# Kernel optimization log

Hardware: AMD Instinct MI355X
Metric: run time of the kernel (lower is better)

Reference implementation:

```python
import jax, jax.numpy as jnp
import numpy as np

N_NODES = 50000


def graph_conv(src, dst, x, W, b, n_nodes):
    """DGL GraphConv, norm='both': D_out^{-1/2} A D_in^{-1/2} x W + b.
    src/dst: [E] edge endpoints (message flows src -> dst).
    """
    ones = jnp.ones(src.shape[0], dtype=x.dtype)
    deg_out = jnp.clip(jax.ops.segment_sum(ones, src, num_segments=n_nodes), 1.0)
    deg_in = jnp.clip(jax.ops.segment_sum(ones, dst, num_segments=n_nodes), 1.0)
    h = x * jax.lax.rsqrt(deg_out)[:, None]          # src-side normalization
    msgs = h[src]                                     # [E, F] gather (irregular)
    agg = jax.ops.segment_sum(msgs, dst, num_segments=n_nodes)  # SpMM scatter-add
    agg = agg * jax.lax.rsqrt(deg_in)[:, None]        # dst-side normalization
    return agg @ W + b


def setup_inputs() -> dict:
    key = jax.random.key(0)
    ks = jax.random.split(key, 9)
    E = 600000
    in_f, hid, emb = 128, 64, 32
    features = jax.random.normal(ks[0], (N_NODES, in_f), dtype=jnp.float32)
    src = jax.random.randint(ks[1], (E,), 0, N_NODES)
    dst = jax.random.randint(ks[2], (E,), 0, N_NODES)

    def glorot(k, fan_in, fan_out):
        lim = np.sqrt(6.0 / (fan_in + fan_out)).astype(np.float32)
        return jax.random.uniform(k, (fan_in, fan_out), jnp.float32, -lim, lim)

    return {
        "features": features, "src": src, "dst": dst,
        "W1": glorot(ks[3], in_f, hid), "b1": jnp.zeros((hid,), jnp.float32),
        "W2": glorot(ks[4], hid, emb), "b2": jnp.zeros((emb,), jnp.float32),
        "W3": glorot(ks[5], emb, in_f), "b3": jnp.zeros((in_f,), jnp.float32),
    }


def reference(features, src, dst, W1, b1, W2, b2, W3, b3):
    h = jax.nn.relu(graph_conv(src, dst, features, W1, b1, N_NODES))
    z = graph_conv(src, dst, h, W2, b2, N_NODES)
    recon = graph_conv(src, dst, z, W3, b3, N_NODES)
    return (z, recon)
```

## Files before the change

kernel.cpp:

```cpp
#include <hip/hip_runtime.h>
#include <hip/hip_bf16.h>


#define HNB 4
#define HPB 64
#define HBIN 12500
typedef unsigned short u16;

__device__ __forceinline__ float bfhi(unsigned u) {
    unsigned v = u & 0xFFFF0000u;
    return __builtin_bit_cast(float, v);
}
__device__ __forceinline__ float bflo(unsigned u) {
    unsigned v = u << 16;
    return __builtin_bit_cast(float, v);
}
__device__ __forceinline__ unsigned f2bf(float f) {
    unsigned u = __builtin_bit_cast(unsigned, f);
    return (u + 0x7FFFu + ((u >> 16) & 1u)) >> 16;
}

__global__ __launch_bounds__(256) void k_hist2(
    const int* __restrict__ src, const int* __restrict__ dst,
    u16* __restrict__ slab, int E, int slice)
{
    __shared__ int h[HBIN];
    const int which = blockIdx.x / (HNB * HPB);
    const int bin   = (blockIdx.x / HPB) % HNB;
    const int p     = blockIdx.x % HPB;
    const int* __restrict__ idx = which ? dst : src;

    for (int i = threadIdx.x; i < HBIN; i += 256) h[i] = 0;
    __syncthreads();

    const int lo  = bin * HBIN;
    const int beg = p * slice;
    const int fin = min(beg + slice, E);
    for (int i = beg + threadIdx.x * 4; i + 3 < fin; i += 1024) {
        const int4 v = *(const int4*)(idx + i);
        int u;
        u = v.x - lo; if ((unsigned)u < (unsigned)HBIN) atomicAdd(&h[u], 1);
        u = v.y - lo; if ((unsigned)u < (unsigned)HBIN) atomicAdd(&h[u], 1);
        u = v.z - lo; if ((unsigned)u < (unsigned)HBIN) atomicAdd(&h[u], 1);
        u = v.w - lo; if ((unsigned)u < (unsigned)HBIN) atomicAdd(&h[u], 1);
    }
    for (int i = beg + ((fin - beg) & ~3) + threadIdx.x; i < fin; i += 256) {
        int u = idx[i] - lo;
        if ((unsigned)u < (unsigned)HBIN) atomicAdd(&h[u], 1);
    }
    __syncthreads();

    unsigned* out = (unsigned*)(slab + (size_t)blockIdx.x * HBIN);
    for (int i = threadIdx.x; i < HBIN / 2; i += 256)
        out[i] = (unsigned)h[2 * i] | ((unsigned)h[2 * i + 1] << 16);
}

__global__ __launch_bounds__(256) void k_reduce_scan(
    u16* __restrict__ slab, float* __restrict__ rs_out, float* __restrict__ rs_in,
    int* __restrict__ partial, int* __restrict__ blocksum, int N)
{
    __shared__ int tmp[256];
    const int tid = threadIdx.x;
    const int i = blockIdx.x * 256 + tid;

    int run = 0;
    if (i < N) {
        const int bin = i / HBIN;
        const int off = i - bin * HBIN;
        const u16* s_src = slab + ((size_t)(bin * HPB)) * HBIN + off;
        u16*       s_dst = slab + ((size_t)((HNB + bin) * HPB)) * HBIN + off;

        int so = 0;
#pragma unroll
        for (int p = 0; p < HPB; ++p) so += s_src[(size_t)p * HBIN];
#pragma unroll
        for (int p = 0; p < HPB; ++p) {
            const int c = s_dst[(size_t)p * HBIN];
            s_dst[(size_t)p * HBIN] = (u16)run;
            run += c;
        }
        rs_out[i] = rsqrtf(fmaxf((float)so, 1.0f));
        rs_in[i]  = rsqrtf(fmaxf((float)run, 1.0f));
    }
    tmp[tid] = run; __syncthreads();
    for (int off = 1; off < 256; off <<= 1) {
        int t = (tid >= off) ? tmp[tid - off] : 0;
        __syncthreads(); tmp[tid] += t; __syncthreads();
    }
    if (i < N) partial[i] = tmp[tid];
    if (tid == 255) blocksum[blockIdx.x] = tmp[255];
}

__global__ void k_scan2(int* __restrict__ blocksum, int nb) {
    __shared__ int tmp[256];
    const int tid = threadIdx.x;
    int v = (tid < nb) ? blocksum[tid] : 0;
    tmp[tid] = v; __syncthreads();
    for (int off = 1; off < 256; off <<= 1) {
        int t = (tid >= off) ? tmp[tid - off] : 0;
        __syncthreads(); tmp[tid] += t; __syncthreads();
    }
    if (tid < nb) blocksum[tid] = tmp[tid];
}

__global__ void k_scan3(const int* __restrict__ partial, const int* __restrict__ blocksum,
                        int* __restrict__ row_ptr, int n) {
    const int i = blockIdx.x * 256 + threadIdx.x;
    if (i < n) {
        const int base = (blockIdx.x > 0) ? blocksum[blockIdx.x - 1] : 0;
        row_ptr[i + 1] = partial[i] + base;
        if (i == 0) row_ptr[0] = 0;
    }
}

__global__ __launch_bounds__(256) void k_fill2(
    const int* __restrict__ src, const int* __restrict__ dst,
    const int* __restrict__ row_ptr, const u16* __restrict__ slab,
    int* __restrict__ csr_src, int E, int slice, int N)
{
    __shared__ int cur[HBIN];
    const int bin = blockIdx.x / HPB;
    const int p   = blockIdx.x % HPB;
    const int lo  = bin * HBIN;

    const u16* part_off = slab + ((size_t)((HNB + bin) * HPB + p)) * HBIN;
    for (int j = threadIdx.x; j < HBIN; j += 256) {
        const int node = lo + j;
        cur[j] = (node < N) ? (row_ptr[node] + (int)part_off[j]) : 0;
    }
    __syncthreads();

    const int beg = p * slice;
    const int fin = min(beg + slice, E);
    for (int i = beg + threadIdx.x * 4; i + 3 < fin; i += 1024) {
        const int4 d = *(const int4*)(dst + i);
        const int4 s = *(const int4*)(src + i);
        int u;
        u = d.x - lo; if ((unsigned)u < (unsigned)HBIN) csr_src[atomicAdd(&cur[u], 1)] = s.x;
        u = d.y - lo; if ((unsigned)u < (unsigned)HBIN) csr_src[atomicAdd(&cur[u], 1)] = s.y;
        u = d.z - lo; if ((unsigned)u < (unsigned)HBIN) csr_src[atomicAdd(&cur[u], 1)] = s.z;
        u = d.w - lo; if ((unsigned)u < (unsigned)HBIN) csr_src[atomicAdd(&cur[u], 1)] = s.w;
    }
    for (int i = beg + ((fin - beg) & ~3) + threadIdx.x; i < fin; i += 256) {
        int u = dst[i] - lo;
        if ((unsigned)u < (unsigned)HBIN) csr_src[atomicAdd(&cur[u], 1)] = src[i];
    }
}

template <int IN_F, int OUT_F, int TM>
__global__ __launch_bounds__(256) void k_gemm_bf16out(
    const float* __restrict__ X, const float* __restrict__ W,
    const float* __restrict__ rowscale, u16* __restrict__ Y, int n)
{
    constexpr int CT  = OUT_F / 4;
    constexpr int RT  = 256 / CT;
    constexpr int RPT = TM / RT;
    constexpr int XS  = IN_F + 4;
    __shared__ float sW[IN_F * OUT_F];
    __shared__ float sX[TM * XS];
    const int tid = threadIdx.x;
    const int row0 = blockIdx.x * TM;

    for (int i = tid; i < IN_F * OUT_F / 4; i += 256)
        ((float4*)sW)[i] = ((const float4*)W)[i];
    for (int i = tid; i < TM * IN_F / 4; i += 256) {
        const int r  = i / (IN_F / 4);
        const int c4 = (i % (IN_F / 4)) * 4;
        const int gr = row0 + r;
        float4 v = make_float4(0.f, 0.f, 0.f, 0.f);
        if (gr < n) v = *(const float4*)(X + (long)gr * IN_F + c4);
        *(float4*)(sX + r * XS + c4) = v;
    }
    __syncthreads();

    const int tc = tid % CT;
    const int tr = tid / CT;
    float4 acc[RPT];
#pragma unroll
    for (int i = 0; i < RPT; ++i) acc[i] = make_float4(0.f, 0.f, 0.f, 0.f);

#pragma unroll 8
    for (int k = 0; k < IN_F; ++k) {
        const float4 w = *(const float4*)(sW + k * OUT_F + 4 * tc);
#pragma unroll
        for (int i = 0; i < RPT; ++i) {
            const float xv = sX[(tr + i * RT) * XS + k];
            acc[i].x += xv * w.x; acc[i].y += xv * w.y;
            acc[i].z += xv * w.z; acc[i].w += xv * w.w;
        }
    }

#pragma unroll
    for (int i = 0; i < RPT; ++i) {
        const int gr = row0 + tr + i * RT;
        if (gr < n) {
            float4 v = acc[i];
            const float s = rowscale[gr];
            v.x *= s; v.y *= s; v.z *= s; v.w *= s;
            uint2 pk;
            pk.x = f2bf(v.x) | (f2bf(v.y) << 16);
            pk.y = f2bf(v.z) | (f2bf(v.w) << 16);
            *(uint2*)(Y + (size_t)gr * OUT_F + 4 * tc) = pk;
        }
    }
}

__global__ __launch_bounds__(256) void k_gather_gemm_B(
    const int* __restrict__ row_ptr, const int* __restrict__ csr_src,
    const u16* __restrict__ t1b, const float* __restrict__ rs_in,
    const float* __restrict__ rs_out, const float* __restrict__ b1,
    const float* __restrict__ W2, u16* __restrict__ t2b, int N)
{
    __shared__ float sh[32][72];
    __shared__ float sW[64 * 32];
    const int tid = threadIdx.x;

    for (int i = tid; i < 64 * 32 / 4; i += 256)
        ((float4*)sW)[i] = ((const float4*)W2)[i];

    const int nloc = tid / 8;
    const int node = blockIdx.x * 32 + nloc;
    const int c8 = (tid % 8) * 8;

    float a[8];
#pragma unroll
    for (int t = 0; t < 8; ++t) a[t] = 0.f;

    if (node < N) {
        const int beg = row_ptr[node];
        const int end = row_ptr[node + 1];
        int j = beg;
        for (; j + 3 < end; j += 4) {
            const int s0 = csr_src[j], s1 = csr_src[j + 1];
            const int s2 = csr_src[j + 2], s3 = csr_src[j + 3];
            const uint4 q0 = *(const uint4*)(t1b + (size_t)s0 * 64 + c8);
            const uint4 q1 = *(const uint4*)(t1b + (size_t)s1 * 64 + c8);
            const uint4 q2 = *(const uint4*)(t1b + (size_t)s2 * 64 + c8);
            const uint4 q3 = *(const uint4*)(t1b + (size_t)s3 * 64 + c8);
            a[0] += bflo(q0.x); a[1] += bfhi(q0.x); a[2] += bflo(q0.y); a[3] += bfhi(q0.y);
            a[4] += bflo(q0.z); a[5] += bfhi(q0.z); a[6] += bflo(q0.w); a[7] += bfhi(q0.w);
            a[0] += bflo(q1.x); a[1] += bfhi(q1.x); a[2] += bflo(q1.y); a[3] += bfhi(q1.y);
            a[4] += bflo(q1.z); a[5] += bfhi(q1.z); a[6] += bflo(q1.w); a[7] += bfhi(q1.w);
            a[0] += bflo(q2.x); a[1] += bfhi(q2.x); a[2] += bflo(q2.y); a[3] += bfhi(q2.y);
            a[4] += bflo(q2.z); a[5] += bfhi(q2.z); a[6] += bflo(q2.w); a[7] += bfhi(q2.w);
            a[0] += bflo(q3.x); a[1] += bfhi(q3.x); a[2] += bflo(q3.y); a[3] += bfhi(q3.y);
            a[4] += bflo(q3.z); a[5] += bfhi(q3.z); a[6] += bflo(q3.w); a[7] += bfhi(q3.w);
        }
        for (; j < end; ++j) {
            const int s = csr_src[j];
            const uint4 q = *(const uint4*)(t1b + (size_t)s * 64 + c8);
            a[0] += bflo(q.x); a[1] += bfhi(q.x); a[2] += bflo(q.y); a[3] += bfhi(q.y);
            a[4] += bflo(q.z); a[5] += bfhi(q.z); a[6] += bflo(q.w); a[7] += bfhi(q.w);
        }
        const float rs = rs_in[node];
#pragma unroll
        for (int t = 0; t < 8; ++t)
            a[t] = fmaxf(a[t] * rs + b1[c8 + t], 0.f);
    }
#pragma unroll
    for (int t = 0; t < 8; ++t) sh[nloc][c8 + t] = a[t];
    __syncthreads();

    const int n2 = tid / 8;
    const int c4 = (tid % 8) * 4;
    float4 acc = make_float4(0.f, 0.f, 0.f, 0.f);
#pragma unroll 8
    for (int k = 0; k < 64; ++k) {
        const float xv = sh[n2][k];
        const float4 w = *(const float4*)(sW + k * 32 + c4);
        acc.x += xv * w.x; acc.y += xv * w.y; acc.z += xv * w.z; acc.w += xv * w.w;
    }
    const int gn = blockIdx.x * 32 + n2;
    if (gn < N) {
        const float s = rs_out[gn];
        uint2 pk;
        pk.x = f2bf(acc.x * s) | (f2bf(acc.y * s) << 16);
        pk.y = f2bf(acc.z * s) | (f2bf(acc.w * s) << 16);
        *(uint2*)(t2b + (size_t)gn * 32 + c4) = pk;
    }
}

__global__ __launch_bounds__(256) void k_gather_C(
    const int* __restrict__ row_ptr, const int* __restrict__ csr_src,
    const u16* __restrict__ t2b, const float* __restrict__ rs_in,
    const float* __restrict__ rs_out, const float* __restrict__ b2,
    float* __restrict__ z, u16* __restrict__ zb, int N)
{
    const int node = blockIdx.x * 64 + threadIdx.x / 4;
    const int c8 = (threadIdx.x % 4) * 8;
    if (node >= N) return;

    const int beg = row_ptr[node];
    const int end = row_ptr[node + 1];
    float a[8];
#pragma unroll
    for (int t = 0; t < 8; ++t) a[t] = 0.f;

    int j = beg;
    for (; j + 3 < end; j += 4) {
        const int s0 = csr_src[j], s1 = csr_src[j + 1];
        const int s2 = csr_src[j + 2], s3 = csr_src[j + 3];
        const uint4 q0 = *(const uint4*)(t2b + (size_t)s0 * 32 + c8);
        const uint4 q1 = *(const uint4*)(t2b + (size_t)s1 * 32 + c8);
        const uint4 q2 = *(const uint4*)(t2b + (size_t)s2 * 32 + c8);
        const uint4 q3 = *(const uint4*)(t2b + (size_t)s3 * 32 + c8);
        a[0] += bflo(q0.x); a[1] += bfhi(q0.x); a[2] += bflo(q0.y); a[3] += bfhi(q0.y);
        a[4] += bflo(q0.z); a[5] += bfhi(q0.z); a[6] += bflo(q0.w); a[7] += bfhi(q0.w);
        a[0] += bflo(q1.x); a[1] += bfhi(q1.x); a[2] += bflo(q1.y); a[3] += bfhi(q1.y);
        a[4] += bflo(q1.z); a[5] += bfhi(q1.z); a[6] += bflo(q1.w); a[7] += bfhi(q1.w);
        a[0] += bflo(q2.x); a[1] += bfhi(q2.x); a[2] += bflo(q2.y); a[3] += bfhi(q2.y);
        a[4] += bflo(q2.z); a[5] += bfhi(q2.z); a[6] += bflo(q2.w); a[7] += bfhi(q2.w);
        a[0] += bflo(q3.x); a[1] += bfhi(q3.x); a[2] += bflo(q3.y); a[3] += bfhi(q3.y);
        a[4] += bflo(q3.z); a[5] += bfhi(q3.z); a[6] += bflo(q3.w); a[7] += bfhi(q3.w);
    }
    for (; j < end; ++j) {
        const int s = csr_src[j];
        const uint4 q = *(const uint4*)(t2b + (size_t)s * 32 + c8);
        a[0] += bflo(q.x); a[1] += bfhi(q.x); a[2] += bflo(q.y); a[3] += bfhi(q.y);
        a[4] += bflo(q.z); a[5] += bfhi(q.z); a[6] += bflo(q.w); a[7] += bfhi(q.w);
    }

    const float rs = rs_in[node];
    float v[8];
#pragma unroll
    for (int t = 0; t < 8; ++t) v[t] = a[t] * rs + b2[c8 + t];

    float* o = z + (size_t)node * 32 + c8;
    *(float4*)(o)     = make_float4(v[0], v[1], v[2], v[3]);
    *(float4*)(o + 4) = make_float4(v[4], v[5], v[6], v[7]);

    const float ss = rs_out[node];
    uint4 pk;
    pk.x = f2bf(v[0] * ss) | (f2bf(v[1] * ss) << 16);
    pk.y = f2bf(v[2] * ss) | (f2bf(v[3] * ss) << 16);
    pk.z = f2bf(v[4] * ss) | (f2bf(v[5] * ss) << 16);
    pk.w = f2bf(v[6] * ss) | (f2bf(v[7] * ss) << 16);
    *(uint4*)(zb + (size_t)node * 32 + c8) = pk;
}

__global__ __launch_bounds__(256) void k_gather_gemm_D(
    const int* __restrict__ row_ptr, const int* __restrict__ csr_src,
    const u16* __restrict__ zb, const float* __restrict__ rs_in,
    const float* __restrict__ W3, const float* __restrict__ b3,
    float* __restrict__ recon, int N)
{
    __shared__ float sa[64][36];
    __shared__ float sW[32 * 128];
    const int tid = threadIdx.x;

    for (int i = tid; i < 32 * 128 / 4; i += 256)
        ((float4*)sW)[i] = ((const float4*)W3)[i];

    const int nloc = tid / 4;
    const int node = blockIdx.x * 64 + nloc;
    const int c8 = (tid % 4) * 8;

    float a[8];
#pragma unroll
    for (int t = 0; t < 8; ++t) a[t] = 0.f;

    if (node < N) {
        const int beg = row_ptr[node];
        const int end = row_ptr[node + 1];
        int j = beg;
        for (; j + 3 < end; j += 4) {
            const int s0 = csr_src[j], s1 = csr_src[j + 1];
            const int s2 = csr_src[j + 2], s3 = csr_src[j + 3];
            const uint4 q0 = *(const uint4*)(zb + (size_t)s0 * 32 + c8);
            const uint4 q1 = *(const uint4*)(zb + (size_t)s1 * 32 + c8);
            const uint4 q2 = *(const uint4*)(zb + (size_t)s2 * 32 + c8);
            const uint4 q3 = *(const uint4*)(zb + (size_t)s3 * 32 + c8);
            a[0] += bflo(q0.x); a[1] += bfhi(q0.x); a[2] += bflo(q0.y); a[3] += bfhi(q0.y);
            a[4] += bflo(q0.z); a[5] += bfhi(q0.z); a[6] += bflo(q0.w); a[7] += bfhi(q0.w);
            a[0] += bflo(q1.x); a[1] += bfhi(q1.x); a[2] += bflo(q1.y); a[3] += bfhi(q1.y);
            a[4] += bflo(q1.z); a[5] += bfhi(q1.z); a[6] += bflo(q1.w); a[7] += bfhi(q1.w);
            a[0] += bflo(q2.x); a[1] += bfhi(q2.x); a[2] += bflo(q2.y); a[3] += bfhi(q2.y);
            a[4] += bflo(q2.z); a[5] += bfhi(q2.z); a[6] += bflo(q2.w); a[7] += bfhi(q2.w);
            a[0] += bflo(q3.x); a[1] += bfhi(q3.x); a[2] += bflo(q3.y); a[3] += bfhi(q3.y);
            a[4] += bflo(q3.z); a[5] += bfhi(q3.z); a[6] += bflo(q3.w); a[7] += bfhi(q3.w);
        }
        for (; j < end; ++j) {
            const int s = csr_src[j];
            const uint4 q = *(const uint4*)(zb + (size_t)s * 32 + c8);
            a[0] += bflo(q.x); a[1] += bfhi(q.x); a[2] += bflo(q.y); a[3] += bfhi(q.y);
            a[4] += bflo(q.z); a[5] += bfhi(q.z); a[6] += bflo(q.w); a[7] += bfhi(q.w);
        }
        const float rs = rs_in[node];
#pragma unroll
        for (int t = 0; t < 8; ++t) a[t] *= rs;
    }
#pragma unroll
    for (int t = 0; t < 8; ++t) sa[nloc][c8 + t] = a[t];
    __syncthreads();

    const int ng = (tid / 32) * 8;
    const int c4 = (tid % 32) * 4;
    const float4 bb = *(const float4*)(b3 + c4);
    float4 acc[8];
#pragma unroll
    for (int i = 0; i < 8; ++i) acc[i] = bb;
#pragma unroll 4
    for (int k = 0; k < 32; ++k) {
        const float4 w = *(const float4*)(sW + k * 128 + c4);
#pragma unroll
        for (int i = 0; i < 8; ++i) {
            const float xv = sa[ng + i][k];
            acc[i].x += xv * w.x; acc[i].y += xv * w.y;
            acc[i].z += xv * w.z; acc[i].w += xv * w.w;
        }
    }
#pragma unroll
    for (int i = 0; i < 8; ++i) {
        const int gn = blockIdx.x * 64 + ng + i;
        if (gn < N) *(float4*)(recon + (size_t)gn * 128 + c4) = acc[i];
    }
}

extern "C" void kernel_launch(void* const* d_in, const int* in_sizes, int n_in,
                              void* d_out, int out_size, void* d_ws, size_t ws_size,
                              hipStream_t stream) {
    const float* feat = (const float*)d_in[0];
    const int*   src  = (const int*)d_in[1];
    const int*   dst  = (const int*)d_in[2];
    const float* W1   = (const float*)d_in[3];
    const float* b1   = (const float*)d_in[4];
    const float* W2   = (const float*)d_in[5];
    const float* b2   = (const float*)d_in[6];
    const float* W3   = (const float*)d_in[7];
    const float* b3   = (const float*)d_in[8];

    const int E = in_sizes[1];
    const int N = in_sizes[0] / 128;
    const int slice = (((E + HPB - 1) / HPB) + 3) & ~3;

    const size_t SLABN = 2UL * HNB * HPB * HBIN;
    u16* slab     = (u16*)d_ws;
    int* row_ptr  = (int*)(slab + SLABN);
    int* scan_p   = row_ptr + N + 16;
    int* blocksum = scan_p + N;
    int* csr_src  = blocksum + 256;
    float* rs_out = (float*)(csr_src + E);
    float* rs_in  = rs_out + N;
    u16* t2b      = (u16*)(rs_in + N);
    u16* zb       = t2b + (size_t)N * 32;
    u16* t1b      = (u16*)slab;

    float* z_out  = (float*)d_out;
    float* recon  = z_out + (size_t)N * 32;

    const int B = 256;
    const int nb_scan = (N + 255) / 256;

    k_hist2<<<2 * HNB * HPB, B, 0, stream>>>(src, dst, slab, E, slice);
    k_reduce_scan<<<nb_scan, B, 0, stream>>>(slab, rs_out, rs_in, scan_p, blocksum, N);
    k_scan2<<<1, B, 0, stream>>>(blocksum, nb_scan);
    k_scan3<<<nb_scan, B, 0, stream>>>(scan_p, blocksum, row_ptr, N);
    k_fill2<<<HNB * HPB, B, 0, stream>>>(src, dst, row_ptr, slab, csr_src, E, slice, N);

    k_gemm_bf16out<128, 64, 32><<<(N + 31) / 32, B, 0, stream>>>(
        feat, W1, rs_out, t1b, N);

    k_gather_gemm_B<<<(N + 31) / 32, B, 0, stream>>>(
        row_ptr, csr_src, t1b, rs_in, rs_out, b1, W2, t2b, N);

    k_gather_C<<<(N + 63) / 64, B, 0, stream>>>(
        row_ptr, csr_src, t2b, rs_in, rs_out, b2, z_out, zb, N);

    k_gather_gemm_D<<<(N + 63) / 64, B, 0, stream>>>(
        row_ptr, csr_src, zb, rs_in, W3, b3, recon, N);
}
```

Measured before the change: 212.7 us.

## Sort nodes by in-degree for balanced gather work and fuse scan kernels

Computes an in-degree histogram during the reduce-scan, builds a degree-bucketed node permutation with a new placement kernel, and has all three gather kernels process nodes in that order. The goal is to cut wavefront divergence from uneven neighbour-list lengths inside a block. It also merges the two scan kernels into one, which removes a launch. The cost is an extra kernel, an extra workspace array, and scattered output writes through the permutation instead of contiguous rows.

After: 217.9 us. +2.4%, slower.

```diff
diff --git a/kernel.cpp b/kernel.cpp
--- a/kernel.cpp
+++ b/kernel.cpp
@@ -5,6 +5,7 @@
 #define HNB 4
 #define HPB 64
 #define HBIN 12500
+#define DB 64
 typedef unsigned short u16;
 
 __device__ __forceinline__ float bfhi(unsigned u) {
@@ -22,9 +23,10 @@
 
 __global__ __launch_bounds__(256) void k_hist2(
     const int* __restrict__ src, const int* __restrict__ dst,
-    u16* __restrict__ slab, int E, int slice)
+    u16* __restrict__ slab, int* __restrict__ degcnt, int E, int slice)
 {
     __shared__ int h[HBIN];
+    if (blockIdx.x == 0 && threadIdx.x < DB) degcnt[threadIdx.x] = 0;
     const int which = blockIdx.x / (HNB * HPB);
     const int bin   = (blockIdx.x / HPB) % HNB;
     const int p     = blockIdx.x % HPB;
@@ -57,11 +59,14 @@
 
 __global__ __launch_bounds__(256) void k_reduce_scan(
     u16* __restrict__ slab, float* __restrict__ rs_out, float* __restrict__ rs_in,
-    int* __restrict__ partial, int* __restrict__ blocksum, int N)
+    int* __restrict__ partial, int* __restrict__ blocksum,
+    int* __restrict__ deg, int* __restrict__ degcnt, int N)
 {
     __shared__ int tmp[256];
+    __shared__ int dh[DB];
     const int tid = threadIdx.x;
     const int i = blockIdx.x * 256 + tid;
+    if (tid < DB) dh[tid] = 0;
 
     int run = 0;
     if (i < N) {
@@ -81,17 +86,25 @@
         }
         rs_out[i] = rsqrtf(fmaxf((float)so, 1.0f));
         rs_in[i]  = rsqrtf(fmaxf((float)run, 1.0f));
+        deg[i] = run;
     }
     tmp[tid] = run; __syncthreads();
+    if (i < N) atomicAdd(&dh[min(run, DB - 1)], 1);
     for (int off = 1; off < 256; off <<= 1) {
         int t = (tid >= off) ? tmp[tid - off] : 0;
         __syncthreads(); tmp[tid] += t; __syncthreads();
     }
     if (i < N) partial[i] = tmp[tid];
     if (tid == 255) blocksum[blockIdx.x] = tmp[255];
-}
-
-__global__ void k_scan2(int* __restrict__ blocksum, int nb) {
+    __syncthreads();
+    if (tid < DB && dh[tid] > 0) atomicAdd(&degcnt[tid], dh[tid]);
+}
+
+__global__ __launch_bounds__(256) void k_scan23(
+    const int* __restrict__ partial, const int* __restrict__ blocksum,
+    int* __restrict__ row_ptr, const int* __restrict__ degcnt,
+    int* __restrict__ degbase, int n, int nb)
+{
     __shared__ int tmp[256];
     const int tid = threadIdx.x;
     int v = (tid < nb) ? blocksum[tid] : 0;
@@ -100,16 +113,17 @@
         int t = (tid >= off) ? tmp[tid - off] : 0;
         __syncthreads(); tmp[tid] += t; __syncthreads();
     }
-    if (tid < nb) blocksum[tid] = tmp[tid];
-}
-
-__global__ void k_scan3(const int* __restrict__ partial, const int* __restrict__ blocksum,
-                        int* __restrict__ row_ptr, int n) {
-    const int i = blockIdx.x * 256 + threadIdx.x;
+    __syncthreads();
+    const int i = blockIdx.x * 256 + tid;
     if (i < n) {
-        const int base = (blockIdx.x > 0) ? blocksum[blockIdx.x - 1] : 0;
+        const int base = (blockIdx.x > 0) ? tmp[blockIdx.x - 1] : 0;
         row_ptr[i + 1] = partial[i] + base;
         if (i == 0) row_ptr[0] = 0;
+    }
+    if (blockIdx.x == 0 && tid == 0) {
+        int run = 0;
+#pragma unroll
+        for (int k = 0; k < DB; ++k) { const int c = degcnt[k]; degbase[k] = run; run += c; }
     }
 }
 
@@ -147,6 +161,27 @@
     }
 }
 
+__global__ __launch_bounds__(256) void k_place(
+    const int* __restrict__ deg, int* __restrict__ cursor,
+    int* __restrict__ perm, int N)
+{
+    __shared__ int lcnt[DB];
+    __shared__ int gb[DB];
+    const int tid = threadIdx.x;
+    const int i = blockIdx.x * 256 + tid;
+    if (tid < DB) lcnt[tid] = 0;
+    __syncthreads();
+    int d = 0, lrank = 0;
+    if (i < N) {
+        d = min(deg[i], DB - 1);
+        lrank = atomicAdd(&lcnt[d], 1);
+    }
+    __syncthreads();
+    if (tid < DB) gb[tid] = (lcnt[tid] > 0) ? atomicAdd(&cursor[tid], lcnt[tid]) : 0;
+    __syncthreads();
+    if (i < N) perm[gb[d] + lrank] = i;
+}
+
 template <int IN_F, int OUT_F, int TM>
 __global__ __launch_bounds__(256) void k_gemm_bf16out(
     const float* __restrict__ X, const float* __restrict__ W,
@@ -206,6 +241,7 @@
 }
 
 __global__ __launch_bounds__(256) void k_gather_gemm_B(
+    const int* __restrict__ perm,
     const int* __restrict__ row_ptr, const int* __restrict__ csr_src,
     const u16* __restrict__ t1b, const float* __restrict__ rs_in,
     const float* __restrict__ rs_out, const float* __restrict__ b1,
@@ -213,20 +249,23 @@
 {
     __shared__ float sh[32][72];
     __shared__ float sW[64 * 32];
+    __shared__ int snode[32];
     const int tid = threadIdx.x;
 
     for (int i = tid; i < 64 * 32 / 4; i += 256)
         ((float4*)sW)[i] = ((const float4*)W2)[i];
 
     const int nloc = tid / 8;
-    const int node = blockIdx.x * 32 + nloc;
+    const int gid = blockIdx.x * 32 + nloc;
+    const int node = (gid < N) ? perm[gid] : -1;
     const int c8 = (tid % 8) * 8;
+    if ((tid & 7) == 0) snode[nloc] = node;
 
     float a[8];
 #pragma unroll
     for (int t = 0; t < 8; ++t) a[t] = 0.f;
 
-    if (node < N) {
+    if (node >= 0) {
         const int beg = row_ptr[node];
         const int end = row_ptr[node + 1];
         int j = beg;
@@ -270,8 +309,8 @@
         const float4 w = *(const float4*)(sW + k * 32 + c4);
         acc.x += xv * w.x; acc.y += xv * w.y; acc.z += xv * w.z; acc.w += xv * w.w;
     }
-    const int gn = blockIdx.x * 32 + n2;
-    if (gn < N) {
+    const int gn = snode[n2];
+    if (gn >= 0) {
         const float s = rs_out[gn];
         uint2 pk;
         pk.x = f2bf(acc.x * s) | (f2bf(acc.y * s) << 16);
@@ -281,14 +320,16 @@
 }
 
 __global__ __launch_bounds__(256) void k_gather_C(
+    const int* __restrict__ perm,
     const int* __restrict__ row_ptr, const int* __restrict__ csr_src,
     const u16* __restrict__ t2b, const float* __restrict__ rs_in,
     const float* __restrict__ rs_out, const float* __restrict__ b2,
     float* __restrict__ z, u16* __restrict__ zb, int N)
 {
-    const int node = blockIdx.x * 64 + threadIdx.x / 4;
+    const int gid = blockIdx.x * 64 + threadIdx.x / 4;
     const int c8 = (threadIdx.x % 4) * 8;
-    if (node >= N) return;
+    if (gid >= N) return;
+    const int node = perm[gid];
 
     const int beg = row_ptr[node];
     const int end = row_ptr[node + 1];
@@ -339,6 +380,7 @@
 }
 
 __global__ __launch_bounds__(256) void k_gather_gemm_D(
+    const int* __restrict__ perm,
     const int* __restrict__ row_ptr, const int* __restrict__ csr_src,
     const u16* __restrict__ zb, const float* __restrict__ rs_in,
     const float* __restrict__ W3, const float* __restrict__ b3,
@@ -346,20 +388,23 @@
 {
     __shared__ float sa[64][36];
     __shared__ float sW[32 * 128];
+    __shared__ int snode[64];
     const int tid = threadIdx.x;
 
     for (int i = tid; i < 32 * 128 / 4; i += 256)
         ((float4*)sW)[i] = ((const float4*)W3)[i];
 
     const int nloc = tid / 4;
-    const int node = blockIdx.x * 64 + nloc;
+    const int gid = blockIdx.x * 64 + nloc;
+    const int node = (gid < N) ? perm[gid] : -1;
     const int c8 = (tid % 4) * 8;
+    if ((tid & 3) == 0) snode[nloc] = node;
 
     float a[8];
 #pragma unroll
     for (int t = 0; t < 8; ++t) a[t] = 0.f;
 
-    if (node < N) {
+    if (node >= 0) {
         const int beg = row_ptr[node];
         const int end = row_ptr[node + 1];
         int j = beg;
@@ -411,8 +456,8 @@
     }
 #pragma unroll
     for (int i = 0; i < 8; ++i) {
-        const int gn = blockIdx.x * 64 + ng + i;
-        if (gn < N) *(float4*)(recon + (size_t)gn * 128 + c4) = acc[i];
+        const int gn = snode[ng + i];
+        if (gn >= 0) *(float4*)(recon + (size_t)gn * 128 + c4) = acc[i];
     }
 }
 
@@ -438,7 +483,11 @@
     int* row_ptr  = (int*)(slab + SLABN);
     int* scan_p   = row_ptr + N + 16;
     int* blocksum = scan_p + N;
-    int* csr_src  = blocksum + 256;
+    int* degcnt   = blocksum + 256;
+    int* degbase  = degcnt + DB;
+    int* deg      = degbase + DB;
+    int* perm     = deg + N;
+    int* csr_src  = perm + N;
     float* rs_out = (float*)(csr_src + E);
     float* rs_in  = rs_out + N;
     u16* t2b      = (u16*)(rs_in + N);
@@ -451,21 +500,23 @@
     const int B = 256;
     const int nb_scan = (N + 255) / 256;
 
-    k_hist2<<<2 * HNB * HPB, B, 0, stream>>>(src, dst, slab, E, slice);
-    k_reduce_scan<<<nb_scan, B, 0, stream>>>(slab, rs_out, rs_in, scan_p, blocksum, N);
-    k_scan2<<<1, B, 0, stream>>>(blocksum, nb_scan);
-    k_scan3<<<nb_scan, B, 0, stream>>>(scan_p, blocksum, row_ptr, N);
+    k_hist2<<<2 * HNB * HPB, B, 0, stream>>>(src, dst, slab, degcnt, E, slice);
+    k_reduce_scan<<<nb_scan, B, 0, stream>>>(slab, rs_out, rs_in, scan_p, blocksum,
+                                             deg, degcnt, N);
+    k_scan23<<<nb_scan, B, 0, stream>>>(scan_p, blocksum, row_ptr, degcnt, degbase,
+                                        N, nb_scan);
     k_fill2<<<HNB * HPB, B, 0, stream>>>(src, dst, row_ptr, slab, csr_src, E, slice, N);
+    k_place<<<nb_scan, B, 0, stream>>>(deg, degbase, perm, N);
 
     k_gemm_bf16out<128, 64, 32><<<(N + 31) / 32, B, 0, stream>>>(
         feat, W1, rs_out, t1b, N);
 
     k_gather_gemm_B<<<(N + 31) / 32, B, 0, stream>>>(
-        row_ptr, csr_src, t1b, rs_in, rs_out, b1, W2, t2b, N);
+        perm, row_ptr, csr_src, t1b, rs_in, rs_out, b1, W2, t2b, N);
 
     k_gather_C<<<(N + 63) / 64, B, 0, stream>>>(
-        row_ptr, csr_src, t2b, rs_in, rs_out, b2, z_out, zb, N);
+        perm, row_ptr, csr_src, t2b, rs_in, rs_out, b2, z_out, zb, N);
 
     k_gather_gemm_D<<<(N + 63) / 64, B, 0, stream>>>(
-        row_ptr, csr_src, zb, rs_in, W3, b3, recon, N);
-}
+        perm, row_ptr, csr_src, zb, rs_in, W3, b3, recon, N);
+}
```
